# Kernel tuning notes

Measured on AMD Instinct MI355X. Metric: run time of the kernel, lower is better.

Reference implementation:

```python
import jax, jax.numpy as jnp
import numpy as np

EPS = 1e-5

def _layernorm(x, gamma, beta):
    # normalize over last (channel) axis, per point
    mu = jnp.mean(x, axis=-1, keepdims=True)
    var = jnp.mean(jnp.square(x - mu), axis=-1, keepdims=True)
    return (x - mu) * jax.lax.rsqrt(var + EPS) * gamma + beta

def setup_inputs() -> dict:
    key = jax.random.key(0)
    ks = jax.random.split(key, 12)
    B, N, C, F = 32, 4096, 3, 1024
    points = jax.random.normal(ks[0], (B, N, C), dtype=jnp.float32)
    mask = jax.random.randint(ks[1], (B, 1, N), 0, 2, dtype=jnp.int32)
    s = 0.05
    return {
        "points": points,
        "mask": mask,
        "w1": jax.random.normal(ks[2], (128, C), dtype=jnp.float32) * s,      # conv1 (no bias)
        "g1": jnp.ones((128,), jnp.float32),                                   # norm1 gamma
        "be1": jnp.zeros((128,), jnp.float32),                                 # norm1 beta
        "w2": jax.random.normal(ks[3], (256, 128), dtype=jnp.float32) * s,     # conv2
        "b2": jax.random.normal(ks[4], (256,), dtype=jnp.float32) * s,
        "w3": jax.random.normal(ks[5], (512, 512), dtype=jnp.float32) * s,     # conv3 (no bias)
        "g2": jnp.ones((512,), jnp.float32),                                   # norm2 gamma
        "be2": jnp.zeros((512,), jnp.float32),                                 # norm2 beta
        "w4": jax.random.normal(ks[6], (F, 512), dtype=jnp.float32) * s,       # conv4
        "b4": jax.random.normal(ks[7], (F,), dtype=jnp.float32) * s,
    }

def reference(points, mask, w1, g1, be1, w2, b2, w3, g2, be2, w4, b4):
    # points: [B, N, C]; mask: [B, 1, N]
    vis = (mask[:, 0, :] != 0).astype(points.dtype)[..., None]  # [B, N, 1]
    # conv1 (1x1, no bias) as point-wise matmul
    h0 = jnp.einsum('bnc,kc->bnk', points, w1)                  # [B, N, 128]
    # masked LayerNorm: LN is per-point over channels, so compute densely and zero invisible points
    h1 = _layernorm(h0, g1, be1) * vis
    h2 = jax.nn.relu(h1)
    h3 = jnp.einsum('bnk,ok->bno', h2, w2) + b2                 # [B, N, 256]
    gmax = jnp.max(h3, axis=1, keepdims=True)                   # [B, 1, 256]
    dist = jnp.concatenate([jnp.broadcast_to(gmax, h3.shape), h3], axis=-1)  # [B, N, 512]
    h4 = jnp.einsum('bno,po->bnp', dist, w3)                    # [B, N, 512]
    h5 = _layernorm(h4, g2, be2) * vis
    h6 = jax.nn.relu(h5)
    h7 = jnp.einsum('bnp,fp->bnf', h6, w4) + b4                 # [B, N, F]
    return jnp.max(h7, axis=1)                                  # [B, F]
```

## Files before the change

### kernel.cpp

```cpp
#include <hip/hip_runtime.h>
#include <stdint.h>

#define LN_EPS 1e-5f

static __device__ __forceinline__ unsigned short f2bf_bits(float f) {
  union { float f; unsigned u; } v; v.f = f;
  unsigned r = v.u + 0x7FFFu + ((v.u >> 16) & 1u);
  return (unsigned short)(r >> 16);
}
static __device__ __forceinline__ float bf2f(unsigned short h) {
  union { unsigned u; float f; } v; v.u = ((unsigned)h) << 16;
  return v.f;
}

typedef __bf16 bf16x8 __attribute__((ext_vector_type(8)));
typedef float floatx4 __attribute__((ext_vector_type(4)));

typedef __attribute__((address_space(1))) unsigned int* gas_ptr;
typedef __attribute__((address_space(3))) unsigned int* las_ptr;
static __device__ __forceinline__ void async_cp16(const void* g, void* l) {
  __builtin_amdgcn_global_load_lds((gas_ptr)g, (las_ptr)l, 16, 0, 0);
}

__global__ __launch_bounds__(256) void perm_kernel(
    const int* __restrict__ mask, int* __restrict__ newrow, int* __restrict__ cnt) {
  const int b = blockIdx.x, t = threadIdx.x;
  const int base = b * 4096 + t * 16;
  int v[16]; int s = 0;
#pragma unroll
  for (int i = 0; i < 16; ++i) { v[i] = (mask[base + i] != 0); s += v[i]; }
  const int lane = t & 63, wv = t >> 6;
  int scan = s;
  for (int o = 1; o < 64; o <<= 1) { int x = __shfl_up(scan, o); if (lane >= o) scan += x; }
  __shared__ int wsum[4], woff[4], stotal;
  if (lane == 63) wsum[wv] = scan;
  __syncthreads();
  if (t == 0) { int a = 0; for (int k = 0; k < 4; ++k) { woff[k] = a; a += wsum[k]; } stotal = a; cnt[b] = a; }
  __syncthreads();
  const int excl = scan - s + woff[wv];
  const int total = stotal;
  int run = 0;
#pragma unroll
  for (int i = 0; i < 16; ++i) {
    const int pos = t * 16 + i;
    const int visBefore = excl + run;
    newrow[b * 4096 + pos] = v[i] ? visBefore : total + (pos - visBefore);
    run += v[i];
  }
}

__global__ __launch_bounds__(256) void conv1_ln_kernel(
    const float* __restrict__ points,
    const float* __restrict__ w1, const float* __restrict__ g1,
    const float* __restrict__ be1, unsigned short* __restrict__ h2,
    const int* __restrict__ newrow, const int* __restrict__ cnt,
    const float* __restrict__ w2, const float* __restrict__ w3,
    const float* __restrict__ w4, unsigned short* __restrict__ w2b,
    unsigned short* __restrict__ w3Rb, unsigned short* __restrict__ w4b) {
  if (blockIdx.x >= 32768) {
    int idx = (blockIdx.x - 32768) * 256 + threadIdx.x;
    if (idx < 32768) {
      w2b[idx] = f2bf_bits(w2[idx]);
    } else if (idx < 32768 + 131072) {
      int t = idx - 32768;
      int p = t >> 8, k = t & 255;
      w3Rb[t] = f2bf_bits(w3[p * 512 + 256 + k]);
    } else {
      int t = idx - 163840;
      w4b[t] = f2bf_bits(w4[t]);
    }
    return;
  }
  const int lane = threadIdx.x & 63;
  const int wv = threadIdx.x >> 6;
  const size_t p = (size_t)blockIdx.x * 4 + wv;
  const int dest = newrow[p];
  const int cntb = cnt[p >> 12];
  const int ceilv = (cntb + 127) & ~127;
  if (dest >= ceilv) return;
  const bool vis = (dest < cntb);
  const float x0 = points[p * 3 + 0];
  const float x1 = points[p * 3 + 1];
  const float x2 = points[p * 3 + 2];
  const int c0 = lane * 2, c1 = c0 + 1;
  float h00 = w1[c0 * 3] * x0 + w1[c0 * 3 + 1] * x1 + w1[c0 * 3 + 2] * x2;
  float h01 = w1[c1 * 3] * x0 + w1[c1 * 3 + 1] * x1 + w1[c1 * 3 + 2] * x2;
  float s = h00 + h01;
  for (int o = 32; o; o >>= 1) s += __shfl_xor(s, o);
  const float mu = s * (1.f / 128.f);
  const float d0 = h00 - mu, d1 = h01 - mu;
  float q = d0 * d0 + d1 * d1;
  for (int o = 32; o; o >>= 1) q += __shfl_xor(q, o);
  const float rs = rsqrtf(q * (1.f / 128.f) + LN_EPS);
  const float y0 = vis ? fmaxf(d0 * rs * g1[c0] + be1[c0], 0.f) : 0.f;
  const float y1 = vis ? fmaxf(d1 * rs * g1[c1] + be1[c1], 0.f) : 0.f;
  union { unsigned u; unsigned short s2[2]; } pk;
  pk.s2[0] = f2bf_bits(y0);
  pk.s2[1] = f2bf_bits(y1);
  const size_t prow = (p & ~(size_t)4095) + (size_t)dest;
  ((unsigned*)h2)[prow * 64 + lane] = pk.u;
}

template <int EPI, int NCT>
__global__ __launch_bounds__(256) void gemm_bt(
    const unsigned short* __restrict__ A, const unsigned short* __restrict__ Bw,
    void* __restrict__ outp, float* __restrict__ outp2,
    const float* __restrict__ extra, const int* __restrict__ cnt,
    int M, int N, int K) {
  __shared__ __align__(16) char smA[2][128 * 64];
  __shared__ __align__(16) char smB[2][128 * 64];
  __shared__ float lmax[2][128];

  const int tid = threadIdx.x;
  const int lane = tid & 63;
  const int w = tid >> 6;
  const int wm = w >> 1, wn = w & 1;

  const int gid = blockIdx.x;
  const int xcd = gid & 7;
  const int slot = gid >> 3;
  const int rowsPerXcd = (M >> 7) >> 3;
  const int rowTile = xcd * rowsPerXcd + slot / NCT;
  const int colTile = slot % NCT;
  const size_t rowBase = (size_t)rowTile * 128;
  const int colBase = colTile * 128;

  const int cntb = cnt[rowBase >> 12];
  const int rb = (int)(rowBase & 4095);
  if (rb >= cntb) {
    if (EPI == 1) return;
    if (EPI == 2) {
      if (tid < 128) outp2[(size_t)rowTile * N + colBase + tid] = 0.f;
      return;
    }
    if (EPI == 3) {
      if (tid < 128) outp2[(size_t)rowTile * N + colBase + tid] = extra[colBase + tid];
      return;
    }
  }

  floatx4 acc[4][4];
  const floatx4 zero = {0.f, 0.f, 0.f, 0.f};
#pragma unroll
  for (int i = 0; i < 4; ++i)
#pragma unroll
    for (int j = 0; j < 4; ++j) acc[i][j] = zero;

  const int rSub = lane >> 2;
  const int cb16 = (lane & 3) * 16;
  const size_t Kb = (size_t)K * 2;
  const char* gA = (const char*)A + (rowBase + (size_t)(w * 32 + rSub)) * Kb + cb16;
  const char* gB = (const char*)Bw + ((size_t)colBase + (size_t)(w * 32 + rSub)) * Kb + cb16;
  char* lA0 = smA[0] + w * 2048;
  char* lA1 = smA[1] + w * 2048;
  char* lB0 = smB[0] + w * 2048;
  char* lB1 = smB[1] + w * 2048;
  const size_t skip16 = 16 * Kb;

  const int fm = lane & 15, fq = lane >> 4;
  const int fOff = fm * 64 + fq * 16;
  const char* pa0 = smA[0] + wm * 64 * 64 + fOff;
  const char* pa1 = smA[1] + wm * 64 * 64 + fOff;
  const char* pb0 = smB[0] + wn * 64 * 64 + fOff;
  const char* pb1 = smB[1] + wn * 64 * 64 + fOff;

  for (int k0 = 0; k0 < K; k0 += 64) {
    async_cp16(gA, lA0);
    async_cp16(gA + skip16, lA0 + 1024);
    async_cp16(gA + 64, lA1);
    async_cp16(gA + 64 + skip16, lA1 + 1024);
    async_cp16(gB, lB0);
    async_cp16(gB + skip16, lB0 + 1024);
    async_cp16(gB + 64, lB1);
    async_cp16(gB + 64 + skip16, lB1 + 1024);
    gA += 128; gB += 128;
    __syncthreads();
    bf16x8 af0[4], bg0[4], af1[4], bg1[4];
#pragma unroll
    for (int i = 0; i < 4; ++i) af0[i] = *(const bf16x8*)(pa0 + i * 16 * 64);
#pragma unroll
    for (int j = 0; j < 4; ++j) bg0[j] = *(const bf16x8*)(pb0 + j * 16 * 64);
#pragma unroll
    for (int i = 0; i < 4; ++i)
#pragma unroll
      for (int j = 0; j < 4; ++j)
        acc[i][j] = __builtin_amdgcn_mfma_f32_16x16x32_bf16(af0[i], bg0[j], acc[i][j], 0, 0, 0);
#pragma unroll
    for (int i = 0; i < 4; ++i) af1[i] = *(const bf16x8*)(pa1 + i * 16 * 64);
#pragma unroll
    for (int j = 0; j < 4; ++j) bg1[j] = *(const bf16x8*)(pb1 + j * 16 * 64);
#pragma unroll
    for (int i = 0; i < 4; ++i)
#pragma unroll
      for (int j = 0; j < 4; ++j)
        acc[i][j] = __builtin_amdgcn_mfma_f32_16x16x32_bf16(af1[i], bg1[j], acc[i][j], 0, 0, 0);
    __syncthreads();
  }

  float m4[4] = {-1e30f, -1e30f, -1e30f, -1e30f};

  if (EPI == 1 || EPI == 3) {
    unsigned short* O = (unsigned short*)outp;
#pragma unroll
    for (int j = 0; j < 4; ++j) {
      const int col = colBase + wn * 64 + j * 16 + fm;
      const float ex = (EPI == 1) ? extra[(rowBase >> 12) * (size_t)N + col] : extra[col];
#pragma unroll
      for (int i = 0; i < 4; ++i) {
        const size_t row0 = rowBase + wm * 64 + i * 16 + fq * 4;
#pragma unroll
        for (int r = 0; r < 4; ++r) {
          const float v = acc[i][j][r] + ex;
          if (EPI == 3) m4[j] = fmaxf(m4[j], v);
          O[(row0 + r) * (size_t)N + col] = f2bf_bits(v);
        }
      }
    }
  } else {
#pragma unroll
    for (int j = 0; j < 4; ++j) {
#pragma unroll
      for (int i = 0; i < 4; ++i)
#pragma unroll
        for (int r = 0; r < 4; ++r) m4[j] = fmaxf(m4[j], acc[i][j][r]);
    }
  }

  if (EPI == 2 || EPI == 3) {
#pragma unroll
    for (int j = 0; j < 4; ++j) {
      m4[j] = fmaxf(m4[j], __shfl_xor(m4[j], 16));
      m4[j] = fmaxf(m4[j], __shfl_xor(m4[j], 32));
    }
    const float sel = (fq == 0) ? m4[0] : (fq == 1) ? m4[1] : (fq == 2) ? m4[2] : m4[3];
    lmax[wm][wn * 64 + fq * 16 + fm] = sel;
    __syncthreads();
    if (tid < 128) {
      const float v = fmaxf(lmax[0][tid], lmax[1][tid]);
      outp2[(size_t)rowTile * N + colBase + tid] = v;
    }
  }
}

__global__ __launch_bounds__(256) void gmax_cvec_kernel(
    const float* __restrict__ pg, const float* __restrict__ w3,
    float* __restrict__ cvec) {
  __shared__ float gm[256];
  const int b = blockIdx.x, t = threadIdx.x;
  float m = -1e30f;
  for (int s = 0; s < 32; ++s) m = fmaxf(m, pg[((size_t)b * 32 + s) * 256 + t]);
  gm[t] = m;
  __syncthreads();
#pragma unroll
  for (int half = 0; half < 2; ++half) {
    const int p = half * 256 + t;
    const float* wr = w3 + (size_t)p * 512;
    float s = 0.f;
    for (int c = 0; c < 256; ++c) s += wr[c] * gm[c];
    cvec[b * 512 + p] = s;
  }
}

__global__ __launch_bounds__(256) void ln2_kernel(
    unsigned short* __restrict__ h46, const int* __restrict__ cnt,
    const float* __restrict__ g2, const float* __restrict__ be2) {
  const int lane = threadIdx.x & 63;
  const int wv = threadIdx.x >> 6;
  const size_t p = (size_t)blockIdx.x * 4 + wv;
  const int cb = cnt[p >> 12];
  const int pin = (int)(p & 4095);
  const int ceilv = (cb + 127) & ~127;
  if (pin >= ceilv) return;
  unsigned short* row = h46 + p * 512;
  const int c0 = lane * 8;
  if (pin >= cb) {
    const uint4 z = {0, 0, 0, 0};
    *(uint4*)(row + c0) = z;
    return;
  }
  union { uint4 v; unsigned short s[8]; } in;
  in.v = *(const uint4*)(row + c0);
  float f[8];
  float s = 0.f;
#pragma unroll
  for (int k = 0; k < 8; ++k) { f[k] = bf2f(in.s[k]); s += f[k]; }
  for (int o = 32; o; o >>= 1) s += __shfl_xor(s, o);
  const float mu = s * (1.f / 512.f);
  float q = 0.f;
#pragma unroll
  for (int k = 0; k < 8; ++k) { const float d = f[k] - mu; q += d * d; }
  for (int o = 32; o; o >>= 1) q += __shfl_xor(q, o);
  const float rs = rsqrtf(q * (1.f / 512.f) + LN_EPS);
  union { uint4 v; unsigned short s[8]; } outv;
#pragma unroll
  for (int k = 0; k < 8; ++k) {
    const float y = fmaxf((f[k] - mu) * rs * g2[c0 + k] + be2[c0 + k], 0.f);
    outv.s[k] = f2bf_bits(y);
  }
  *(uint4*)(row + c0) = outv.v;
}

__global__ __launch_bounds__(256) void final_kernel(
    const float* __restrict__ pmax, const float* __restrict__ b4,
    float* __restrict__ out) {
  const int idx = blockIdx.x * 256 + threadIdx.x;
  const int b = idx >> 10, f = idx & 1023;
  float m = -1e30f;
  for (int r = 0; r < 32; ++r) m = fmaxf(m, pmax[((size_t)(b * 32 + r)) * 1024 + f]);
  out[idx] = m + b4[f];
}

extern "C" void kernel_launch(void* const* d_in, const int* in_sizes, int n_in,
                              void* d_out, int out_size, void* d_ws, size_t ws_size,
                              hipStream_t stream) {
  const float* points = (const float*)d_in[0];
  const int* mask = (const int*)d_in[1];
  const float* w1 = (const float*)d_in[2];
  const float* g1 = (const float*)d_in[3];
  const float* be1 = (const float*)d_in[4];
  const float* w2 = (const float*)d_in[5];
  const float* b2 = (const float*)d_in[6];
  const float* w3 = (const float*)d_in[7];
  const float* g2 = (const float*)d_in[8];
  const float* be2 = (const float*)d_in[9];
  const float* w4 = (const float*)d_in[10];
  const float* b4 = (const float*)d_in[11];
  float* out = (float*)d_out;
  char* ws = (char*)d_ws;

  const size_t OFF_H46 = 0;
  const size_t OFF_H2 = 0;
  const size_t OFF_H3 = 134217728;
  const size_t OFF_W2B = OFF_H3 + 67108864;
  const size_t OFF_W3RB = OFF_W2B + 65536;
  const size_t OFF_W4B = OFF_W3RB + 262144;
  const size_t OFF_PG = OFF_W4B + 1048576;
  const size_t OFF_CVEC = OFF_PG + 1048576;
  const size_t OFF_PMAX = OFF_CVEC + 65536;
  const size_t OFF_CNT = OFF_PMAX + 4194304;
  const size_t OFF_NEWROW = OFF_CNT + 4096;

  unsigned short* h2 = (unsigned short*)(ws + OFF_H2);
  unsigned short* h3 = (unsigned short*)(ws + OFF_H3);
  unsigned short* h46 = (unsigned short*)(ws + OFF_H46);
  unsigned short* w2b = (unsigned short*)(ws + OFF_W2B);
  unsigned short* w3Rb = (unsigned short*)(ws + OFF_W3RB);
  unsigned short* w4b = (unsigned short*)(ws + OFF_W4B);
  float* pg = (float*)(ws + OFF_PG);
  float* cvecp = (float*)(ws + OFF_CVEC);
  float* pmaxp = (float*)(ws + OFF_PMAX);
  int* cntp = (int*)(ws + OFF_CNT);
  int* newrow = (int*)(ws + OFF_NEWROW);

  perm_kernel<<<32, 256, 0, stream>>>(mask, newrow, cntp);
  conv1_ln_kernel<<<32768 + 2688, 256, 0, stream>>>(points, w1, g1, be1, h2,
                                                    newrow, cntp, w2, w3, w4, w2b, w3Rb, w4b);
  gemm_bt<3, 2><<<2048, 256, 0, stream>>>(h2, w2b, (void*)h3, pg, b2, cntp, 131072, 256, 128);
  gmax_cvec_kernel<<<32, 256, 0, stream>>>(pg, w3, cvecp);
  gemm_bt<1, 4><<<4096, 256, 0, stream>>>(h3, w3Rb, (void*)h46, nullptr, cvecp, cntp, 131072, 512, 256);
  ln2_kernel<<<32768, 256, 0, stream>>>(h46, cntp, g2, be2);
  gemm_bt<2, 8><<<8192, 256, 0, stream>>>(h46, w4b, nullptr, pmaxp, nullptr, cntp, 131072, 1024, 512);
  final_kernel<<<128, 256, 0, stream>>>(pmaxp, b4, out);
}
```

Baseline: 282.1 us.

## Fold conv2 into conv3 weights to skip materializing h3

Precomputes a combined weight w23 = w3[:,256:] @ w2 plus a bias vector w3[:,256:] @ b2, so the conv3 GEMM reads h2 with K=128 instead of reading a materialized h3 with K=256. The conv2 GEMM now only computes the per-tile column max (plus bias) and no longer writes h3. The per-batch global-max contribution (cvec) moves from the conv3 GEMM epilogue into the LN2 kernel. This removes a large bf16 write and read of h3 and halves the K of the conv3 GEMM. In exchange it adds a small precompute and changes rounding, since w23 is rounded to bf16 after an fp32 product.

```diff
diff --git a/kernel.cpp b/kernel.cpp
--- a/kernel.cpp
+++ b/kernel.cpp
@@ -54,20 +54,29 @@
     const float* __restrict__ w1, const float* __restrict__ g1,
     const float* __restrict__ be1, unsigned short* __restrict__ h2,
     const int* __restrict__ newrow, const int* __restrict__ cnt,
-    const float* __restrict__ w2, const float* __restrict__ w3,
-    const float* __restrict__ w4, unsigned short* __restrict__ w2b,
-    unsigned short* __restrict__ w3Rb, unsigned short* __restrict__ w4b) {
+    const float* __restrict__ w2, const float* __restrict__ b2,
+    const float* __restrict__ w3, const float* __restrict__ w4,
+    unsigned short* __restrict__ w2b, unsigned short* __restrict__ w4b,
+    unsigned short* __restrict__ w23b, float* __restrict__ vecb) {
   if (blockIdx.x >= 32768) {
-    int idx = (blockIdx.x - 32768) * 256 + threadIdx.x;
-    if (idx < 32768) {
-      w2b[idx] = f2bf_bits(w2[idx]);
-    } else if (idx < 32768 + 131072) {
-      int t = idx - 32768;
-      int p = t >> 8, k = t & 255;
-      w3Rb[t] = f2bf_bits(w3[p * 512 + 256 + k]);
+    const int bb = blockIdx.x - 32768;
+    if (bb < 2176) {
+      int idx = bb * 256 + threadIdx.x;
+      if (idx < 32768) w2b[idx] = f2bf_bits(w2[idx]);
+      else w4b[idx - 32768] = f2bf_bits(w4[idx - 32768]);
     } else {
-      int t = idx - 163840;
-      w4b[t] = f2bf_bits(w4[t]);
+      const int tid = threadIdx.x;
+      const int p = (bb - 2176) * 2 + (tid >> 7);
+      const int c = tid & 127;
+      const float* w3r = w3 + (size_t)p * 512 + 256;
+      float s = 0.f;
+      for (int k = 0; k < 256; ++k) s += w3r[k] * w2[k * 128 + c];
+      w23b[p * 128 + c] = f2bf_bits(s);
+      if (c == 0) {
+        float vb = 0.f;
+        for (int k = 0; k < 256; ++k) vb += w3r[k] * b2[k];
+        vecb[p] = vb;
+      }
     }
     return;
   }
@@ -128,12 +137,12 @@
   const int cntb = cnt[rowBase >> 12];
   const int rb = (int)(rowBase & 4095);
   if (rb >= cntb) {
-    if (EPI == 1) return;
+    if (EPI == 0) return;
     if (EPI == 2) {
       if (tid < 128) outp2[(size_t)rowTile * N + colBase + tid] = 0.f;
       return;
     }
-    if (EPI == 3) {
+    if (EPI == 4) {
       if (tid < 128) outp2[(size_t)rowTile * N + colBase + tid] = extra[colBase + tid];
       return;
     }
@@ -199,34 +208,40 @@
 
   float m4[4] = {-1e30f, -1e30f, -1e30f, -1e30f};
 
-  if (EPI == 1 || EPI == 3) {
+  if (EPI == 0) {
     unsigned short* O = (unsigned short*)outp;
 #pragma unroll
     for (int j = 0; j < 4; ++j) {
       const int col = colBase + wn * 64 + j * 16 + fm;
-      const float ex = (EPI == 1) ? extra[(rowBase >> 12) * (size_t)N + col] : extra[col];
+      const float ex = extra[col];
 #pragma unroll
       for (int i = 0; i < 4; ++i) {
         const size_t row0 = rowBase + wm * 64 + i * 16 + fq * 4;
 #pragma unroll
         for (int r = 0; r < 4; ++r) {
-          const float v = acc[i][j][r] + ex;
-          if (EPI == 3) m4[j] = fmaxf(m4[j], v);
-          O[(row0 + r) * (size_t)N + col] = f2bf_bits(v);
+          O[(row0 + r) * (size_t)N + col] = f2bf_bits(acc[i][j][r] + ex);
         }
       }
     }
+  } else if (EPI == 2) {
+#pragma unroll
+    for (int j = 0; j < 4; ++j)
+#pragma unroll
+      for (int i = 0; i < 4; ++i)
+#pragma unroll
+        for (int r = 0; r < 4; ++r) m4[j] = fmaxf(m4[j], acc[i][j][r]);
   } else {
 #pragma unroll
     for (int j = 0; j < 4; ++j) {
+      const float ex = extra[colBase + wn * 64 + j * 16 + fm];
 #pragma unroll
       for (int i = 0; i < 4; ++i)
 #pragma unroll
-        for (int r = 0; r < 4; ++r) m4[j] = fmaxf(m4[j], acc[i][j][r]);
-    }
-  }
-
-  if (EPI == 2 || EPI == 3) {
+        for (int r = 0; r < 4; ++r) m4[j] = fmaxf(m4[j], acc[i][j][r] + ex);
+    }
+  }
+
+  if (EPI == 2 || EPI == 4) {
 #pragma unroll
     for (int j = 0; j < 4; ++j) {
       m4[j] = fmaxf(m4[j], __shfl_xor(m4[j], 16));
@@ -263,6 +278,7 @@
 
 __global__ __launch_bounds__(256) void ln2_kernel(
     unsigned short* __restrict__ h46, const int* __restrict__ cnt,
+    const float* __restrict__ cvec,
     const float* __restrict__ g2, const float* __restrict__ be2) {
   const int lane = threadIdx.x & 63;
   const int wv = threadIdx.x >> 6;
@@ -278,12 +294,16 @@
     *(uint4*)(row + c0) = z;
     return;
   }
+  const int b = (int)(p >> 12);
   union { uint4 v; unsigned short s[8]; } in;
   in.v = *(const uint4*)(row + c0);
+  float cv[8];
+  *(float4*)(cv) = *(const float4*)(cvec + b * 512 + c0);
+  *(float4*)(cv + 4) = *(const float4*)(cvec + b * 512 + c0 + 4);
   float f[8];
   float s = 0.f;
 #pragma unroll
-  for (int k = 0; k < 8; ++k) { f[k] = bf2f(in.s[k]); s += f[k]; }
+  for (int k = 0; k < 8; ++k) { f[k] = bf2f(in.s[k]) + cv[k]; s += f[k]; }
   for (int o = 32; o; o >>= 1) s += __shfl_xor(s, o);
   const float mu = s * (1.f / 512.f);
   float q = 0.f;
@@ -329,23 +349,23 @@
   char* ws = (char*)d_ws;
 
   const size_t OFF_H46 = 0;
-  const size_t OFF_H2 = 0;
-  const size_t OFF_H3 = 134217728;
-  const size_t OFF_W2B = OFF_H3 + 67108864;
-  const size_t OFF_W3RB = OFF_W2B + 65536;
-  const size_t OFF_W4B = OFF_W3RB + 262144;
-  const size_t OFF_PG = OFF_W4B + 1048576;
+  const size_t OFF_H2 = 134217728;
+  const size_t OFF_W2B = OFF_H2 + 33554432;
+  const size_t OFF_W4B = OFF_W2B + 65536;
+  const size_t OFF_W23B = OFF_W4B + 1048576;
+  const size_t OFF_VECB = OFF_W23B + 131072;
+  const size_t OFF_PG = OFF_VECB + 2048;
   const size_t OFF_CVEC = OFF_PG + 1048576;
   const size_t OFF_PMAX = OFF_CVEC + 65536;
   const size_t OFF_CNT = OFF_PMAX + 4194304;
   const size_t OFF_NEWROW = OFF_CNT + 4096;
 
   unsigned short* h2 = (unsigned short*)(ws + OFF_H2);
-  unsigned short* h3 = (unsigned short*)(ws + OFF_H3);
   unsigned short* h46 = (unsigned short*)(ws + OFF_H46);
   unsigned short* w2b = (unsigned short*)(ws + OFF_W2B);
-  unsigned short* w3Rb = (unsigned short*)(ws + OFF_W3RB);
   unsigned short* w4b = (unsigned short*)(ws + OFF_W4B);
+  unsigned short* w23b = (unsigned short*)(ws + OFF_W23B);
+  float* vecb = (float*)(ws + OFF_VECB);
   float* pg = (float*)(ws + OFF_PG);
   float* cvecp = (float*)(ws + OFF_CVEC);
   float* pmaxp = (float*)(ws + OFF_PMAX);
@@ -353,12 +373,12 @@
   int* newrow = (int*)(ws + OFF_NEWROW);
 
   perm_kernel<<<32, 256, 0, stream>>>(mask, newrow, cntp);
-  conv1_ln_kernel<<<32768 + 2688, 256, 0, stream>>>(points, w1, g1, be1, h2,
-                                                    newrow, cntp, w2, w3, w4, w2b, w3Rb, w4b);
-  gemm_bt<3, 2><<<2048, 256, 0, stream>>>(h2, w2b, (void*)h3, pg, b2, cntp, 131072, 256, 128);
+  conv1_ln_kernel<<<32768 + 2176 + 256, 256, 0, stream>>>(
+      points, w1, g1, be1, h2, newrow, cntp, w2, b2, w3, w4, w2b, w4b, w23b, vecb);
+  gemm_bt<4, 2><<<2048, 256, 0, stream>>>(h2, w2b, nullptr, pg, b2, cntp, 131072, 256, 128);
   gmax_cvec_kernel<<<32, 256, 0, stream>>>(pg, w3, cvecp);
-  gemm_bt<1, 4><<<4096, 256, 0, stream>>>(h3, w3Rb, (void*)h46, nullptr, cvecp, cntp, 131072, 512, 256);
-  ln2_kernel<<<32768, 256, 0, stream>>>(h46, cntp, g2, be2);
+  gemm_bt<0, 4><<<4096, 256, 0, stream>>>(h2, w23b, (void*)h46, nullptr, vecb, cntp, 131072, 512, 128);
+  ln2_kernel<<<32768, 256, 0, stream>>>(h46, cntp, cvecp, g2, be2);
   gemm_bt<2, 8><<<8192, 256, 0, stream>>>(h46, w4b, nullptr, pmaxp, nullptr, cntp, 131072, 1024, 512);
   final_kernel<<<128, 256, 0, stream>>>(pmaxp, b4, out);
 }
```

Result: no change. 283.8 us (+0.6%).
